# Kernel tuning notes

Hardware: AMD Instinct MI355X
Metric: run time of the kernel (lower is better)

The kernel has to match this reference:

```python
import jax, jax.numpy as jnp
import numpy as np

B, DIM, HEADS, H, W = 2, 256, 8, 40, 40


def setup_inputs() -> dict:
    key = jax.random.key(0)
    ks = jax.random.split(key, 11)
    s = 0.05
    return {
        "x": jax.random.normal(ks[0], (B, DIM, H, W), jnp.float32),
        "qkv_w": jax.random.normal(ks[1], (3 * DIM, DIM, 1, 1), jnp.float32) * s,
        "qkv_b": jax.random.normal(ks[2], (3 * DIM,), jnp.float32) * s,
        "pos_w": jax.random.normal(ks[3], (3 * DIM, 1, 3, 3), jnp.float32) * s,
        "pos_b": jax.random.normal(ks[4], (3 * DIM,), jnp.float32) * s,
        "proj_w": jax.random.normal(ks[5], (DIM, DIM), jnp.float32) * s,
        "proj_b": jax.random.normal(ks[6], (DIM,), jnp.float32) * s,
        "g1_w": jax.random.normal(ks[7], (16, 1), jnp.float32),
        "g1_b": jax.random.normal(ks[8], (16,), jnp.float32),
        "g2_w": jax.random.normal(ks[9], (1, 16), jnp.float32),
        "g2_b": jax.random.normal(ks[10], (1,), jnp.float32),
    }


def _conv(x, w, b, groups=1, pad=0):
    # NCHW conv, OIHW weights (matches torch Conv2d)
    y = jax.lax.conv_general_dilated(x, w, (1, 1), [(pad, pad), (pad, pad)],
                                     feature_group_count=groups)
    return y + b[None, :, None, None]


def reference(x, qkv_w, qkv_b, pos_w, pos_b, proj_w, proj_b, g1_w, g1_b, g2_w, g2_b):
    b, c, h, w = x.shape
    n = h * w
    hd = c // HEADS
    scale = hd ** -0.5

    qkv = _conv(x, qkv_w, qkv_b)                     # [b, 3c, h, w]
    qkv = _conv(qkv, pos_w, pos_b, groups=3 * c, pad=1)  # depthwise 3x3
    q, k, v = jnp.split(qkv, 3, axis=1)

    def to_heads(t):  # [b,c,h,w] -> [b, heads, n, head_dim]
        return t.reshape(b, HEADS, hd, n).transpose(0, 1, 3, 2)

    q, k, v = to_heads(q), to_heads(k), to_heads(v)

    attn = jnp.einsum('bhnd,bhmd->bhnm', q, k) * scale      # [b,H,n,n]
    prob = jax.nn.softmax(attn, axis=-1)
    entropy = -(prob * jnp.log(jnp.clip(prob, 1e-12))).sum(-1).mean(-1)  # [b,H]

    # EntropyGate: ratio in [0.1, 1.0]
    hid = jax.nn.relu(entropy[..., None] @ g1_w.T + g1_b)
    ratio = jax.nn.sigmoid(hid @ g2_w.T + g2_b)[..., 0] * 0.9 + 0.1      # [b,H]

    # dynamic per-(b,head) top-k: keep = ceil(ratio*n), clamped to [1,n]
    keep = jnp.clip(jnp.ceil(ratio * n).astype(jnp.int32), 1, n)          # [b,H]
    srt = jnp.flip(jnp.sort(attn, axis=-1), axis=-1)                      # descending
    idx = jnp.broadcast_to((keep - 1)[:, :, None, None], (b, HEADS, n, 1))
    kth = jnp.take_along_axis(srt, idx, axis=-1)                          # [b,H,n,1]
    sparse = jnp.where(attn >= kth, attn, -jnp.inf)

    p = jax.nn.softmax(sparse, axis=-1)
    out = jnp.einsum('bhnm,bhmd->bhnd', p, v)
    out = out.transpose(0, 2, 1, 3).reshape(b, n, c)
    out = out @ proj_w.T + proj_b
    return out.transpose(0, 2, 1).reshape(b, c, h, w)
```

## Files before the change

### kernel.cpp

```cpp
#include <hip/hip_runtime.h>
#include <math.h>

#define BB 2
#define CDIM 256
#define NHEADS 8
#define HD 32
#define HH 40
#define WW 40
#define NN 1600
#define C3 768
#define SCALE 0.17677669529663687f
#define RTE 8
#define RTS 2
#define TSTR 2048
#define HSTR 51200

__device__ inline unsigned fkey(float f) {
    unsigned u = __float_as_uint(f);
    return (u & 0x80000000u) ? ~u : (u | 0x80000000u);
}
__device__ inline float finv(unsigned u) {
    unsigned v = (u & 0x80000000u) ? (u ^ 0x80000000u) : ~u;
    return __uint_as_float(v);
}

__global__ __launch_bounds__(256) void conv1x1_kernel(const float* __restrict__ x,
                                                      const float* __restrict__ w,
                                                      const float* __restrict__ bias,
                                                      float* __restrict__ out) {
    int blk = blockIdx.x;
    int st = blk % 7;
    int t2 = blk / 7;
    int ocg = t2 % (C3 / 8);
    int b = t2 / (C3 / 8);
    int s = st * 256 + threadIdx.x;
    if (s >= NN) return;
    int oc0 = ocg * 8;
    const float* xb = x + (size_t)b * CDIM * NN + s;
    const float* w0 = w + (size_t)oc0 * CDIM;
    float a[8];
#pragma unroll
    for (int i = 0; i < 8; i++) a[i] = bias[oc0 + i];
#pragma unroll 4
    for (int ic = 0; ic < CDIM; ic++) {
        float xv = xb[(size_t)ic * NN];
#pragma unroll
        for (int i = 0; i < 8; i++) a[i] += w0[i * CDIM + ic] * xv;
    }
    float* ob = out + ((size_t)b * C3 + oc0) * NN + s;
#pragma unroll
    for (int i = 0; i < 8; i++) ob[(size_t)i * NN] = a[i];
}

__global__ __launch_bounds__(256) void dwconv_kernel(const float* __restrict__ in,
                                                     const float* __restrict__ w,
                                                     const float* __restrict__ bias,
                                                     float* __restrict__ out_t) {
    int idx = blockIdx.x * 256 + threadIdx.x;
    int s = idx % NN;
    int t = idx / NN;
    int c = t % C3;
    int b = t / C3;
    int y = s / WW, xx = s % WW;
    const float* ib = in + ((size_t)b * C3 + c) * NN;
    const float* wr = w + (size_t)c * 9;
    float acc = bias[c];
#pragma unroll
    for (int ky = 0; ky < 3; ky++) {
        int iy = y + ky - 1;
        if (iy < 0 || iy >= HH) continue;
#pragma unroll
        for (int kx = 0; kx < 3; kx++) {
            int ix = xx + kx - 1;
            if (ix < 0 || ix >= WW) continue;
            acc += wr[ky * 3 + kx] * ib[iy * WW + ix];
        }
    }
    int part = c >> 8;
    int r = c & 255;
    int hh = r >> 5;
    int d = r & 31;
    out_t[((size_t)(b * 3 + part) * NHEADS + hh) * HSTR + (s >> 6) * TSTR + d * 64 + (s & 63)] = acc;
}

template <int PERSIST>
__global__ __launch_bounds__(256) void entropy_kernel(const float* __restrict__ qkv_t,
                                                      float* __restrict__ ent,
                                                      float* __restrict__ attw) {
    int blk = blockIdx.x;
    int rt = blk % (NN / RTE);
    int bh = blk / (NN / RTE);
    int h = bh % NHEADS, b = bh / NHEADS;
    int row0 = rt * RTE;
    __shared__ float Qs[RTE][HD];
    int tid = threadIdx.x;
    const float* qt = qkv_t + ((size_t)(b * 3 + 0) * NHEADS + h) * HSTR;
    const float* ktb = qkv_t + ((size_t)(b * 3 + 1) * NHEADS + h) * HSTR;
    {
        int r = tid >> 5, d = tid & 31;
        int row = row0 + r;
        Qs[r][d] = qt[(row >> 6) * TSTR + d * 64 + (row & 63)];
    }
    __syncthreads();
    int w = tid >> 6, lane = tid & 63;
    int lr0 = 2 * w, lr1 = lr0 + 1;
    float* aw0 = nullptr;
    float* aw1 = nullptr;
    if (PERSIST) {
        aw0 = attw + ((size_t)bh * NN + row0 + lr0) * NN;
        aw1 = aw0 + NN;
    }
    float q0[HD], q1[HD];
#pragma unroll
    for (int d = 0; d < HD; d++) { q0[d] = Qs[lr0][d]; q1[d] = Qs[lr1][d]; }
    float S0 = 0.f, T0 = 0.f, S1 = 0.f, T1 = 0.f;
#pragma unroll 1
    for (int kt = 0; kt < 25; kt++) {
        const float* kp = ktb + kt * TSTR + lane;
        float a0 = 0.f, a1 = 0.f;
#pragma unroll
        for (int dc = 0; dc < 4; dc++) {
            float kc[8];
#pragma unroll
            for (int i = 0; i < 8; i++) kc[i] = kp[(dc * 8 + i) * 64];
#pragma unroll
            for (int i = 0; i < 8; i++) {
                a0 += q0[dc * 8 + i] * kc[i];
                a1 += q1[dc * 8 + i] * kc[i];
            }
        }
        a0 *= SCALE; a1 *= SCALE;
        if (PERSIST) {
            int j = kt * 64 + lane;
            aw0[j] = a0;
            aw1[j] = a1;
        }
        float e0 = __expf(a0), e1 = __expf(a1);
        S0 += e0; T0 += e0 * a0;
        S1 += e1; T1 += e1 * a1;
    }
#pragma unroll
    for (int o = 1; o < 64; o <<= 1) {
        S0 += __shfl_xor(S0, o); T0 += __shfl_xor(T0, o);
        S1 += __shfl_xor(S1, o); T1 += __shfl_xor(T1, o);
    }
    if (lane == 0) {
        ent[(size_t)bh * NN + row0 + lr0] = logf(S0) - T0 / S0;
        ent[(size_t)bh * NN + row0 + lr1] = logf(S1) - T1 / S1;
    }
}

__global__ void gate_kernel(const float* __restrict__ ent_rows,
                            const float* __restrict__ g1w, const float* __restrict__ g1b,
                            const float* __restrict__ g2w, const float* __restrict__ g2b,
                            int* __restrict__ keep) {
    int bh = blockIdx.x;
    int tid = threadIdx.x;
    __shared__ float red[4];
    float ls = 0.f;
    for (int j = tid; j < NN; j += 256) ls += ent_rows[bh * NN + j];
    for (int o = 32; o > 0; o >>= 1) ls += __shfl_down(ls, o);
    int lane = tid & 63, wid = tid >> 6;
    if (lane == 0) red[wid] = ls;
    __syncthreads();
    if (tid == 0) {
        float ent = (red[0] + red[1] + red[2] + red[3]) / (float)NN;
        float val = g2b[0];
#pragma unroll
        for (int j = 0; j < 16; j++) {
            float hid = ent * g1w[j] + g1b[j];
            if (hid < 0.f) hid = 0.f;
            val += hid * g2w[j];
        }
        float ratio = 0.9f / (1.f + expf(-val)) + 0.1f;
        int kp = (int)ceilf(ratio * (float)NN);
        if (kp < 1) kp = 1;
        if (kp > NN) kp = NN;
        keep[bh] = kp;
    }
}

template <int PERSIST>
__global__ __launch_bounds__(64) void sparse_attn_kernel(const float* __restrict__ qkv_t,
                                                         const int* __restrict__ keep,
                                                         const float* __restrict__ attbuf,
                                                         float* __restrict__ oht) {
    int blk = blockIdx.x;
    int rt = blk % (NN / RTS);
    int bh = blk / (NN / RTS);
    int h = bh % NHEADS, b = bh / NHEADS;
    int row0 = rt * RTS;
    __shared__ float att[RTS][NN];
    __shared__ unsigned hist[RTS][256];
    __shared__ float Qs[RTS][HD];
    int tid = threadIdx.x;
    const float* ktb = qkv_t + ((size_t)(b * 3 + 1) * NHEADS + h) * HSTR;
    const float* vtb = qkv_t + ((size_t)(b * 3 + 2) * NHEADS + h) * HSTR;
    int want = keep[bh];
    int lane = tid;
    float m0 = -1e30f, m1 = -1e30f;

    if (PERSIST) {
        const float* ab0 = attbuf + ((size_t)bh * NN + row0) * NN;
        const float* ab1 = ab0 + NN;
#pragma unroll 1
        for (int kt = 0; kt < 25; kt++) {
            int j = kt * 64 + lane;
            float a0 = ab0[j];
            float a1 = ab1[j];
            att[0][j] = a0;
            att[1][j] = a1;
            m0 = fmaxf(m0, a0); m1 = fmaxf(m1, a1);
        }
    } else {
        const float* qt = qkv_t + ((size_t)(b * 3 + 0) * NHEADS + h) * HSTR;
        {
            int r = tid >> 5, d = tid & 31;
            int row = row0 + r;
            Qs[r][d] = qt[(row >> 6) * TSTR + d * 64 + (row & 63)];
        }
        __syncthreads();
        float q0[HD], q1[HD];
#pragma unroll
        for (int d = 0; d < HD; d++) { q0[d] = Qs[0][d]; q1[d] = Qs[1][d]; }
#pragma unroll 1
        for (int kt = 0; kt < 25; kt++) {
            const float* kp = ktb + kt * TSTR + lane;
            int j = kt * 64 + lane;
            float kc[HD];
#pragma unroll
            for (int d = 0; d < HD; d++) kc[d] = kp[d * 64];
            float a0 = 0.f, a1 = 0.f;
#pragma unroll
            for (int d = 0; d < HD; d++) { a0 += q0[d] * kc[d]; a1 += q1[d] * kc[d]; }
            a0 *= SCALE; a1 *= SCALE;
            att[0][j] = a0;
            att[1][j] = a1;
            m0 = fmaxf(m0, a0); m1 = fmaxf(m1, a1);
        }
    }
#pragma unroll
    for (int off = 1; off < 64; off <<= 1) {
        m0 = fmaxf(m0, __shfl_xor(m0, off));
        m1 = fmaxf(m1, __shfl_xor(m1, off));
    }

    int l = lane & 31;
    int r = (lane < 32) ? 0 : 1;
    unsigned kvr[50];
#pragma unroll
    for (int k2 = 0; k2 < 50; k2++) kvr[k2] = fkey(att[r][k2 * 32 + l]);

    unsigned prefixHigh = 0;
    for (int pass = 0; pass < 4; pass++) {
        int shift = 24 - 8 * pass;
#pragma unroll
        for (int i = 0; i < 8; i++) hist[r][248 - 8 * l + i] = 0u;
#pragma unroll
        for (int k2 = 0; k2 < 50; k2++) {
            unsigned u = kvr[k2];
            bool ok = (pass == 0) || ((u >> (shift + 8)) == prefixHigh);
            if (ok) atomicAdd(&hist[r][(u >> shift) & 255u], 1u);
        }
        unsigned sch = 0;
#pragma unroll
        for (int i = 0; i < 8; i++) sch += hist[r][248 - 8 * l + i];
        unsigned inc = sch;
#pragma unroll
        for (int dlt = 1; dlt < 32; dlt <<= 1) {
            unsigned tv = __shfl_up(inc, dlt, 32);
            if (l >= dlt) inc += tv;
        }
        unsigned pref = inc - sch;
        bool found = (pref < (unsigned)want) && ((unsigned)want <= inc);
        int bsel = -1, wnew = 0;
        if (found) {
            unsigned want2 = (unsigned)want - pref, cum = 0;
#pragma unroll
            for (int i = 0; i < 8; i++) {
                int bbin = 255 - 8 * l - i;
                unsigned c = hist[r][bbin];
                if (bsel < 0 && cum + c >= want2) { bsel = bbin; wnew = (int)(want2 - cum); }
                cum += c;
            }
        }
        unsigned long long mk = __ballot(found);
        int src = (lane < 32) ? __builtin_ctzll(mk & 0xffffffffULL)
                              : __builtin_ctzll(mk >> 32) + 32;
        bsel = __shfl(bsel, src);
        want = __shfl(wnew, src);
        prefixHigh = (prefixHigh << 8) | (unsigned)bsel;
    }
    float kth = finv(prefixHigh);
    float kth0 = __shfl(kth, 0);
    float kth1 = __shfl(kth, 32);

    float acc0[HD], acc1[HD];
#pragma unroll
    for (int d = 0; d < HD; d++) { acc0[d] = 0.f; acc1[d] = 0.f; }
    float S0 = 0.f, S1 = 0.f;
    for (int kt = 0; kt < 25; kt++) {
        const float* vp = vtb + kt * TSTR + lane;
        int j = kt * 64 + lane;
        float a0 = att[0][j];
        float a1 = att[1][j];
        float p0 = (a0 >= kth0) ? __expf(a0 - m0) : 0.f;
        float p1 = (a1 >= kth1) ? __expf(a1 - m1) : 0.f;
        S0 += p0; S1 += p1;
#pragma unroll
        for (int d = 0; d < HD; d++) {
            float vv = vp[d * 64];
            acc0[d] += p0 * vv;
            acc1[d] += p1 * vv;
        }
    }
#pragma unroll
    for (int off = 1; off < 64; off <<= 1) {
        S0 += __shfl_xor(S0, off);
        S1 += __shfl_xor(S1, off);
    }

    float* scratch = &att[0][0];
    int dd = lane & 31;
    int jb = (lane < 32) ? 0 : 32;
#pragma unroll
    for (int d = 0; d < HD; d++) scratch[lane * 33 + d] = acc0[d];
    float sum0 = 0.f;
#pragma unroll
    for (int jj = 0; jj < 32; jj++) sum0 += scratch[(jb + jj) * 33 + dd];
    sum0 += __shfl_xor(sum0, 32);
#pragma unroll
    for (int d = 0; d < HD; d++) scratch[lane * 33 + d] = acc1[d];
    float sum1 = 0.f;
#pragma unroll
    for (int jj = 0; jj < 32; jj++) sum1 += scratch[(jb + jj) * 33 + dd];
    sum1 += __shfl_xor(sum1, 32);

    if (lane < 32) {
        size_t base = ((size_t)b * CDIM + h * HD + dd) * NN + row0;
        oht[base + 0] = sum0 / S0;
        oht[base + 1] = sum1 / S1;
    }
}

__global__ __launch_bounds__(256) void proj_kernel(const float* __restrict__ oht,
                                                   const float* __restrict__ pw,
                                                   const float* __restrict__ pb,
                                                   float* __restrict__ out) {
    int blk = blockIdx.x;
    int st = blk % 7;
    int t2 = blk / 7;
    int ocg = t2 % (CDIM / 8);
    int b = t2 / (CDIM / 8);
    int s = st * 256 + threadIdx.x;
    if (s >= NN) return;
    int co0 = ocg * 8;
    const float* ib = oht + (size_t)b * CDIM * NN + s;
    const float* w0 = pw + (size_t)co0 * CDIM;
    float a[8];
#pragma unroll
    for (int i = 0; i < 8; i++) a[i] = pb[co0 + i];
#pragma unroll 4
    for (int c = 0; c < CDIM; c++) {
        float xv = ib[(size_t)c * NN];
#pragma unroll
        for (int i = 0; i < 8; i++) a[i] += w0[i * CDIM + c] * xv;
    }
    float* ob = out + ((size_t)b * CDIM + co0) * NN + s;
#pragma unroll
    for (int i = 0; i < 8; i++) ob[(size_t)i * NN] = a[i];
}

extern "C" void kernel_launch(void* const* d_in, const int* in_sizes, int n_in,
                              void* d_out, int out_size, void* d_ws, size_t ws_size,
                              hipStream_t stream) {
    const float* x      = (const float*)d_in[0];
    const float* qkv_w  = (const float*)d_in[1];
    const float* qkv_b  = (const float*)d_in[2];
    const float* pos_w  = (const float*)d_in[3];
    const float* pos_b  = (const float*)d_in[4];
    const float* proj_w = (const float*)d_in[5];
    const float* proj_b = (const float*)d_in[6];
    const float* g1w    = (const float*)d_in[7];
    const float* g1b    = (const float*)d_in[8];
    const float* g2w    = (const float*)d_in[9];
    const float* g2b    = (const float*)d_in[10];
    float* out = (float*)d_out;

    float* ws   = (float*)d_ws;
    float* buf1 = ws;
    float* buf2 = buf1 + (size_t)BB * C3 * NN;
    float* ent  = buf2 + (size_t)BB * C3 * NN;
    float* oht  = ent + (size_t)BB * NHEADS * NN;
    int* keep   = (int*)(oht + (size_t)BB * CDIM * NN);
    float* attbuf = (float*)(keep + 16);
    size_t need = (size_t)((char*)(attbuf + (size_t)BB * NHEADS * NN * NN) - (char*)d_ws);
    bool persist = (ws_size >= need);

    conv1x1_kernel<<<BB * (C3 / 8) * 7, 256, 0, stream>>>(x, qkv_w, qkv_b, buf1);
    dwconv_kernel<<<BB * C3 * NN / 256, 256, 0, stream>>>(buf1, pos_w, pos_b, buf2);
    if (persist) {
        entropy_kernel<1><<<NHEADS * BB * (NN / RTE), 256, 0, stream>>>(buf2, ent, attbuf);
        gate_kernel<<<BB * NHEADS, 256, 0, stream>>>(ent, g1w, g1b, g2w, g2b, keep);
        sparse_attn_kernel<1><<<NHEADS * BB * (NN / RTS), 64, 0, stream>>>(buf2, keep, attbuf, oht);
    } else {
        entropy_kernel<0><<<NHEADS * BB * (NN / RTE), 256, 0, stream>>>(buf2, ent, nullptr);
        gate_kernel<<<BB * NHEADS, 256, 0, stream>>>(ent, g1w, g1b, g2w, g2b, keep);
        sparse_attn_kernel<0><<<NHEADS * BB * (NN / RTS), 64, 0, stream>>>(buf2, keep, nullptr, oht);
    }
    proj_kernel<<<BB * (CDIM / 8) * 7, 256, 0, stream>>>(oht, proj_w, proj_b, out);
}
```

Before: 421.1 us.

## Split persistent sparse attention into separate top-k select and PV kernels

When the cached attention buffer fits, the fused 64-thread kernel that did the radix top-k selection and the PV accumulation is replaced by two 256-thread kernels. The first reads scores from global memory straight into registers, computes the row max and kth threshold, and writes both per row. The second rereads the scores and V to accumulate the output. This drops the large per-block shared score array and aims to raise occupancy, at the cost of reading the score matrix from global memory twice plus one extra launch.

```diff
diff --git a/kernel.cpp b/kernel.cpp
--- a/kernel.cpp
+++ b/kernel.cpp
@@ -180,10 +180,156 @@
     }
 }
 
-template <int PERSIST>
+__global__ __launch_bounds__(256, 4) void select_kernel(const float* __restrict__ attbuf,
+                                                        const int* __restrict__ keep,
+                                                        float* __restrict__ kth_out,
+                                                        float* __restrict__ m_out) {
+    int blk = blockIdx.x;
+    int rt = blk % (NN / 8);
+    int bh = blk / (NN / 8);
+    int row0 = rt * 8;
+    __shared__ unsigned hist[4][RTS][256];
+    int tid = threadIdx.x;
+    int wv = tid >> 6;
+    int lane = tid & 63;
+    int wrow0 = row0 + 2 * wv;
+    int want = keep[bh];
+    int l = lane & 31;
+    int r = (lane < 32) ? 0 : 1;
+    const float* ar = attbuf + ((size_t)bh * NN + wrow0 + r) * NN;
+
+    unsigned kvr[50];
+#pragma unroll
+    for (int k2 = 0; k2 < 50; k2++) kvr[k2] = fkey(ar[k2 * 32 + l]);
+
+    unsigned mk = 0u;
+#pragma unroll
+    for (int k2 = 0; k2 < 50; k2++) mk = mk > kvr[k2] ? mk : kvr[k2];
+#pragma unroll
+    for (int off = 1; off < 32; off <<= 1) {
+        unsigned o = (unsigned)__shfl_xor((int)mk, off);
+        mk = mk > o ? mk : o;
+    }
+
+    unsigned prefixHigh = 0;
+    for (int pass = 0; pass < 4; pass++) {
+        int shift = 24 - 8 * pass;
+#pragma unroll
+        for (int i = 0; i < 8; i++) hist[wv][r][248 - 8 * l + i] = 0u;
+#pragma unroll
+        for (int k2 = 0; k2 < 50; k2++) {
+            unsigned u = kvr[k2];
+            bool ok = (pass == 0) || ((u >> (shift + 8)) == prefixHigh);
+            if (ok) atomicAdd(&hist[wv][r][(u >> shift) & 255u], 1u);
+        }
+        unsigned sch = 0;
+#pragma unroll
+        for (int i = 0; i < 8; i++) sch += hist[wv][r][248 - 8 * l + i];
+        unsigned inc = sch;
+#pragma unroll
+        for (int dlt = 1; dlt < 32; dlt <<= 1) {
+            unsigned tv = __shfl_up(inc, dlt, 32);
+            if (l >= dlt) inc += tv;
+        }
+        unsigned pref = inc - sch;
+        bool found = (pref < (unsigned)want) && ((unsigned)want <= inc);
+        int bsel = -1, wnew = 0;
+        if (found) {
+            unsigned want2 = (unsigned)want - pref, cum = 0;
+#pragma unroll
+            for (int i = 0; i < 8; i++) {
+                int bbin = 255 - 8 * l - i;
+                unsigned c = hist[wv][r][bbin];
+                if (bsel < 0 && cum + c >= want2) { bsel = bbin; wnew = (int)(want2 - cum); }
+                cum += c;
+            }
+        }
+        unsigned long long mkb = __ballot(found);
+        int src = (lane < 32) ? __builtin_ctzll(mkb & 0xffffffffULL)
+                              : __builtin_ctzll(mkb >> 32) + 32;
+        bsel = __shfl(bsel, src);
+        want = __shfl(wnew, src);
+        prefixHigh = (prefixHigh << 8) | (unsigned)bsel;
+    }
+    if (l == 0) {
+        kth_out[(size_t)bh * NN + wrow0 + r] = finv(prefixHigh);
+        m_out[(size_t)bh * NN + wrow0 + r] = finv(mk);
+    }
+}
+
+__global__ __launch_bounds__(256, 4) void pv_kernel(const float* __restrict__ qkv_t,
+                                                    const float* __restrict__ attbuf,
+                                                    const float* __restrict__ kth_in,
+                                                    const float* __restrict__ m_in,
+                                                    float* __restrict__ oht) {
+    int blk = blockIdx.x;
+    int rt = blk % (NN / 8);
+    int bh = blk / (NN / 8);
+    int h = bh % NHEADS, b = bh / NHEADS;
+    int row0 = rt * 8;
+    __shared__ float scratch[4][64 * 33];
+    int tid = threadIdx.x;
+    int wv = tid >> 6;
+    int lane = tid & 63;
+    int r0 = row0 + 2 * wv;
+    const float* vtb = qkv_t + ((size_t)(b * 3 + 2) * NHEADS + h) * HSTR;
+    const float* ab0 = attbuf + ((size_t)bh * NN + r0) * NN;
+    const float* ab1 = ab0 + NN;
+    float m0 = m_in[(size_t)bh * NN + r0];
+    float m1 = m_in[(size_t)bh * NN + r0 + 1];
+    float kth0 = kth_in[(size_t)bh * NN + r0];
+    float kth1 = kth_in[(size_t)bh * NN + r0 + 1];
+
+    float acc0[HD], acc1[HD];
+#pragma unroll
+    for (int d = 0; d < HD; d++) { acc0[d] = 0.f; acc1[d] = 0.f; }
+    float S0 = 0.f, S1 = 0.f;
+    for (int kt = 0; kt < 25; kt++) {
+        const float* vp = vtb + kt * TSTR + lane;
+        int j = kt * 64 + lane;
+        float a0 = ab0[j];
+        float a1 = ab1[j];
+        float p0 = (a0 >= kth0) ? __expf(a0 - m0) : 0.f;
+        float p1 = (a1 >= kth1) ? __expf(a1 - m1) : 0.f;
+        S0 += p0; S1 += p1;
+#pragma unroll
+        for (int d = 0; d < HD; d++) {
+            float vv = vp[d * 64];
+            acc0[d] += p0 * vv;
+            acc1[d] += p1 * vv;
+        }
+    }
+#pragma unroll
+    for (int off = 1; off < 64; off <<= 1) {
+        S0 += __shfl_xor(S0, off);
+        S1 += __shfl_xor(S1, off);
+    }
+
+    float* sc = &scratch[wv][0];
+    int dd = lane & 31;
+    int jb = (lane < 32) ? 0 : 32;
+#pragma unroll
+    for (int d = 0; d < HD; d++) sc[lane * 33 + d] = acc0[d];
+    float sum0 = 0.f;
+#pragma unroll
+    for (int jj = 0; jj < 32; jj++) sum0 += sc[(jb + jj) * 33 + dd];
+    sum0 += __shfl_xor(sum0, 32);
+#pragma unroll
+    for (int d = 0; d < HD; d++) sc[lane * 33 + d] = acc1[d];
+    float sum1 = 0.f;
+#pragma unroll
+    for (int jj = 0; jj < 32; jj++) sum1 += sc[(jb + jj) * 33 + dd];
+    sum1 += __shfl_xor(sum1, 32);
+
+    if (lane < 32) {
+        size_t base = ((size_t)b * CDIM + h * HD + dd) * NN + r0;
+        oht[base + 0] = sum0 / S0;
+        oht[base + 1] = sum1 / S1;
+    }
+}
+
 __global__ __launch_bounds__(64) void sparse_attn_kernel(const float* __restrict__ qkv_t,
                                                          const int* __restrict__ keep,
-                                                         const float* __restrict__ attbuf,
                                                          float* __restrict__ oht) {
     int blk = blockIdx.x;
     int rt = blk % (NN / RTS);
@@ -194,63 +340,45 @@
     __shared__ unsigned hist[RTS][256];
     __shared__ float Qs[RTS][HD];
     int tid = threadIdx.x;
+    const float* qt = qkv_t + ((size_t)(b * 3 + 0) * NHEADS + h) * HSTR;
     const float* ktb = qkv_t + ((size_t)(b * 3 + 1) * NHEADS + h) * HSTR;
     const float* vtb = qkv_t + ((size_t)(b * 3 + 2) * NHEADS + h) * HSTR;
+    {
+        int r = tid >> 5, d = tid & 31;
+        int row = row0 + r;
+        Qs[r][d] = qt[(row >> 6) * TSTR + d * 64 + (row & 63)];
+    }
     int want = keep[bh];
+    __syncthreads();
     int lane = tid;
+    float q0[HD], q1[HD];
+#pragma unroll
+    for (int d = 0; d < HD; d++) { q0[d] = Qs[0][d]; q1[d] = Qs[1][d]; }
     float m0 = -1e30f, m1 = -1e30f;
-
-    if (PERSIST) {
-        const float* ab0 = attbuf + ((size_t)bh * NN + row0) * NN;
-        const float* ab1 = ab0 + NN;
-#pragma unroll 1
-        for (int kt = 0; kt < 25; kt++) {
-            int j = kt * 64 + lane;
-            float a0 = ab0[j];
-            float a1 = ab1[j];
-            att[0][j] = a0;
-            att[1][j] = a1;
-            m0 = fmaxf(m0, a0); m1 = fmaxf(m1, a1);
-        }
-    } else {
-        const float* qt = qkv_t + ((size_t)(b * 3 + 0) * NHEADS + h) * HSTR;
-        {
-            int r = tid >> 5, d = tid & 31;
-            int row = row0 + r;
-            Qs[r][d] = qt[(row >> 6) * TSTR + d * 64 + (row & 63)];
-        }
-        __syncthreads();
-        float q0[HD], q1[HD];
-#pragma unroll
-        for (int d = 0; d < HD; d++) { q0[d] = Qs[0][d]; q1[d] = Qs[1][d]; }
-#pragma unroll 1
-        for (int kt = 0; kt < 25; kt++) {
-            const float* kp = ktb + kt * TSTR + lane;
-            int j = kt * 64 + lane;
-            float kc[HD];
-#pragma unroll
-            for (int d = 0; d < HD; d++) kc[d] = kp[d * 64];
-            float a0 = 0.f, a1 = 0.f;
-#pragma unroll
-            for (int d = 0; d < HD; d++) { a0 += q0[d] * kc[d]; a1 += q1[d] * kc[d]; }
-            a0 *= SCALE; a1 *= SCALE;
-            att[0][j] = a0;
-            att[1][j] = a1;
-            m0 = fmaxf(m0, a0); m1 = fmaxf(m1, a1);
-        }
+    for (int kt = 0; kt < 25; kt++) {
+        const float* kp = ktb + kt * TSTR + lane;
+        int j = kt * 64 + lane;
+        float kc[HD];
+#pragma unroll
+        for (int d = 0; d < HD; d++) kc[d] = kp[d * 64];
+        float a0 = 0.f, a1 = 0.f;
+#pragma unroll
+        for (int d = 0; d < HD; d++) { a0 += q0[d] * kc[d]; a1 += q1[d] * kc[d]; }
+        a0 *= SCALE; a1 *= SCALE;
+        att[0][j] = a0;
+        att[1][j] = a1;
+        m0 = fmaxf(m0, a0); m1 = fmaxf(m1, a1);
     }
 #pragma unroll
     for (int off = 1; off < 64; off <<= 1) {
         m0 = fmaxf(m0, __shfl_xor(m0, off));
         m1 = fmaxf(m1, __shfl_xor(m1, off));
     }
-
     int l = lane & 31;
     int r = (lane < 32) ? 0 : 1;
     unsigned kvr[50];
 #pragma unroll
     for (int k2 = 0; k2 < 50; k2++) kvr[k2] = fkey(att[r][k2 * 32 + l]);
-
     unsigned prefixHigh = 0;
     for (int pass = 0; pass < 4; pass++) {
         int shift = 24 - 8 * pass;
@@ -294,7 +422,6 @@
     float kth = finv(prefixHigh);
     float kth0 = __shfl(kth, 0);
     float kth1 = __shfl(kth, 32);
-
     float acc0[HD], acc1[HD];
 #pragma unroll
     for (int d = 0; d < HD; d++) { acc0[d] = 0.f; acc1[d] = 0.f; }
@@ -319,7 +446,6 @@
         S0 += __shfl_xor(S0, off);
         S1 += __shfl_xor(S1, off);
     }
-
     float* scratch = &att[0][0];
     int dd = lane & 31;
     int jb = (lane < 32) ? 0 : 32;
@@ -335,7 +461,6 @@
 #pragma unroll
     for (int jj = 0; jj < 32; jj++) sum1 += scratch[(jb + jj) * 33 + dd];
     sum1 += __shfl_xor(sum1, 32);
-
     if (lane < 32) {
         size_t base = ((size_t)b * CDIM + h * HD + dd) * NN + row0;
         oht[base + 0] = sum0 / S0;
@@ -393,7 +518,9 @@
     float* ent  = buf2 + (size_t)BB * C3 * NN;
     float* oht  = ent + (size_t)BB * NHEADS * NN;
     int* keep   = (int*)(oht + (size_t)BB * CDIM * NN);
-    float* attbuf = (float*)(keep + 16);
+    float* kth  = (float*)(keep + 16);
+    float* mrow = kth + (size_t)BB * NHEADS * NN;
+    float* attbuf = mrow + (size_t)BB * NHEADS * NN;
     size_t need = (size_t)((char*)(attbuf + (size_t)BB * NHEADS * NN * NN) - (char*)d_ws);
     bool persist = (ws_size >= need);
 
@@ -402,11 +529,12 @@
     if (persist) {
         entropy_kernel<1><<<NHEADS * BB * (NN / RTE), 256, 0, stream>>>(buf2, ent, attbuf);
         gate_kernel<<<BB * NHEADS, 256, 0, stream>>>(ent, g1w, g1b, g2w, g2b, keep);
-        sparse_attn_kernel<1><<<NHEADS * BB * (NN / RTS), 64, 0, stream>>>(buf2, keep, attbuf, oht);
+        select_kernel<<<NHEADS * BB * (NN / 8), 256, 0, stream>>>(attbuf, keep, kth, mrow);
+        pv_kernel<<<NHEADS * BB * (NN / 8), 256, 0, stream>>>(buf2, attbuf, kth, mrow, oht);
     } else {
         entropy_kernel<0><<<NHEADS * BB * (NN / RTE), 256, 0, stream>>>(buf2, ent, nullptr);
         gate_kernel<<<BB * NHEADS, 256, 0, stream>>>(ent, g1w, g1b, g2w, g2b, keep);
-        sparse_attn_kernel<0><<<NHEADS * BB * (NN / RTS), 64, 0, stream>>>(buf2, keep, nullptr, oht);
+        sparse_attn_kernel<<<NHEADS * BB * (NN / RTS), 64, 0, stream>>>(buf2, keep, oht);
     }
     proj_kernel<<<BB * (CDIM / 8) * 7, 256, 0, stream>>>(oht, proj_w, proj_b, out);
 }
```

New measurement: 419.7 us. No clear change (-0.3%).
